# Performance work log

Hardware: AMD Instinct MI355X
Metric: run time of the kernel (lower is better)

Reference implementation:

```python
import jax, jax.numpy as jnp
import numpy as np

DIM = 1280
NUM_HEADS = 16
HEAD_DIM = DIM // NUM_HEADS  # 80
SCALE = HEAD_DIM ** -0.5
N_CHUNKS = 4
CHUNK = 2048
TOTAL = N_CHUNKS * CHUNK  # 8192


def setup_inputs() -> dict:
    key = jax.random.key(0)
    ks = jax.random.split(key, 5)
    hidden_states = jax.random.normal(ks[0], (TOTAL, DIM), dtype=jnp.float32)
    cu_seqlens = (jnp.arange(N_CHUNKS + 1, dtype=jnp.int32) * CHUNK)
    qkv_w = jax.random.normal(ks[1], (3 * DIM, DIM), dtype=jnp.float32) * (DIM ** -0.5)
    qkv_b = jax.random.normal(ks[2], (3 * DIM,), dtype=jnp.float32) * 0.02
    proj_w = jax.random.normal(ks[3], (DIM, DIM), dtype=jnp.float32) * (DIM ** -0.5)
    proj_b = jax.random.normal(ks[4], (DIM,), dtype=jnp.float32) * 0.02
    return {"hidden_states": hidden_states, "cu_seqlens": cu_seqlens,
            "qkv_w": qkv_w, "qkv_b": qkv_b, "proj_w": proj_w, "proj_b": proj_b}


def reference(hidden_states, cu_seqlens, qkv_w, qkv_b, proj_w, proj_b):
    S = hidden_states.shape[0]
    # fused QKV projection: (S, 3*dim) -> q,k,v each (S, H, Dh)
    qkv = hidden_states @ qkv_w.T + qkv_b
    qkv = qkv.reshape(S, 3, NUM_HEADS, HEAD_DIM)
    q, k, v = qkv[:, 0], qkv[:, 1], qkv[:, 2]
    # chunk boundaries are static metadata (module calls .tolist() on them)
    cu = np.asarray(cu_seqlens)
    outs = []
    for s, e in zip(cu[:-1], cu[1:]):
        s, e = int(s), int(e)
        qc = q[s:e].transpose(1, 0, 2)  # (H, L, Dh)
        kc = k[s:e].transpose(1, 0, 2)
        vc = v[s:e].transpose(1, 0, 2)
        # full (non-causal) attention within the chunk; softmax in fp32
        logits = jnp.einsum('hqd,hkd->hqk', qc, kc) * SCALE
        w = jax.nn.softmax(logits.astype(jnp.float32), axis=-1).astype(qc.dtype)
        oc = jnp.einsum('hqk,hkd->hqd', w, vc)  # (H, L, Dh)
        outs.append(oc.transpose(1, 0, 2).reshape(e - s, DIM))
    attn_out = jnp.concatenate(outs, axis=0)  # (S, dim)
    return attn_out @ proj_w.T + proj_b
```

## Files before the change

kernel.cpp:

```cpp
#include <hip/hip_runtime.h>
#include <hip/hip_bf16.h>
#include <stdint.h>

#define NHEADS 16
#define HDIM 80
#define CHUNK 2048
#define QSCALE 0.11180339887498949f
#define L2E 1.4426950408889634f

typedef __bf16 bf16x8 __attribute__((ext_vector_type(8)));
typedef float f32x4 __attribute__((ext_vector_type(4)));

__device__ __forceinline__ unsigned short f2bf(float f) {
  union { float f; unsigned u; } x; x.f = f;
  unsigned r = (x.u + 0x7fffu + ((x.u >> 16) & 1u)) >> 16;
  return (unsigned short)r;
}

__device__ __forceinline__ float fexp2(float x) {
  float r;
  asm("v_exp_f32 %0, %1" : "=v"(r) : "v"(x));
  return r;
}

__device__ __forceinline__ void gload16(const void* g, void* lds) {
  __builtin_amdgcn_global_load_lds((const __attribute__((address_space(1))) void*)g,
                                   (__attribute__((address_space(3))) void*)lds, 16, 0, 0);
}

__global__ __launch_bounds__(256) void cvt_f32_bf16(const float* __restrict__ in,
                                                    unsigned short* __restrict__ out, int n4) {
  int i = blockIdx.x * 256 + threadIdx.x;
  int stride = gridDim.x * 256;
  for (; i < n4; i += stride) {
    float4 v = reinterpret_cast<const float4*>(in)[i];
    ushort4 o;
    o.x = f2bf(v.x); o.y = f2bf(v.y); o.z = f2bf(v.z); o.w = f2bf(v.w);
    reinterpret_cast<ushort4*>(out)[i] = o;
  }
}

__global__ __launch_bounds__(256) void gemm_bt(
    const unsigned short* __restrict__ A, const unsigned short* __restrict__ B,
    const float* __restrict__ bias, unsigned short* __restrict__ C,
    float* __restrict__ Cf,
    int M, int N, int K, int lda, int scaleN, float scaleVal)
{
  __shared__ unsigned short Ash[128 * 32];
  __shared__ unsigned short Bsh[128 * 32];
  const int tid = threadIdx.x;
  const int lane = tid & 63;
  const int w = tid >> 6;
  const int wr = w >> 1, wc = w & 1;
  const int l15 = lane & 15, lq = lane >> 4;
  const long bm = (long)blockIdx.y * 128;
  const long bn = (long)blockIdx.x * 128;

  f32x4 acc[4][4];
#pragma unroll
  for (int i = 0; i < 4; i++)
#pragma unroll
    for (int j = 0; j < 4; j++) acc[i][j] = f32x4{0.f, 0.f, 0.f, 0.f};

  const int srow = lane >> 2;
  const int scol = (lane & 3) * 8;

  for (long k0 = 0; k0 < K; k0 += 32) {
    __syncthreads();
#pragma unroll
    for (int i = 0; i < 2; i++) {
      gload16(A + (bm + w * 32 + i * 16 + srow) * (long)lda + k0 + scol,
              (char*)Ash + (w * 2 + i) * 1024);
      gload16(B + (bn + w * 32 + i * 16 + srow) * (long)K + k0 + scol,
              (char*)Bsh + (w * 2 + i) * 1024);
    }
    __syncthreads();
    bf16x8 af[4], bfr[4];
#pragma unroll
    for (int x = 0; x < 4; x++) {
      af[x]  = *reinterpret_cast<const bf16x8*>(Ash + (wr * 64 + x * 16 + l15) * 32 + lq * 8);
      bfr[x] = *reinterpret_cast<const bf16x8*>(Bsh + (wc * 64 + x * 16 + l15) * 32 + lq * 8);
    }
#pragma unroll
    for (int x = 0; x < 4; x++)
#pragma unroll
      for (int y = 0; y < 4; y++)
        acc[x][y] = __builtin_amdgcn_mfma_f32_16x16x32_bf16(af[x], bfr[y], acc[x][y], 0, 0, 0);
  }

#pragma unroll
  for (int x = 0; x < 4; x++) {
    long row0 = bm + wr * 64 + x * 16 + lq * 4;
#pragma unroll
    for (int y = 0; y < 4; y++) {
      int col = (int)bn + wc * 64 + y * 16 + l15;
      float bs = bias[col];
      float sc = (col < scaleN) ? scaleVal : 1.0f;
      if (Cf != nullptr) {
#pragma unroll
        for (int r = 0; r < 4; r++)
          Cf[(size_t)(row0 + r) * N + col] = (acc[x][y][r] + bs) * sc;
      } else {
#pragma unroll
        for (int r = 0; r < 4; r++)
          C[(size_t)(row0 + r) * N + col] = f2bf((acc[x][y][r] + bs) * sc);
      }
    }
  }
}

__global__ __launch_bounds__(256) void transpose_v(
    const unsigned short* __restrict__ qkv, unsigned short* __restrict__ vt)
{
  __shared__ unsigned short Tsh[64 * 88];
  const int tid = threadIdx.x;
  const int ch = blockIdx.y >> 4, head = blockIdx.y & 15;
  const int st = blockIdx.x;
  const unsigned short* src = qkv + (size_t)(ch * CHUNK + st * 64) * 3840 + 2560 + head * HDIM;
  for (int s = tid; s < 640; s += 256) {
    int r = s / 10, c = s % 10;
    uint4 v = *reinterpret_cast<const uint4*>(src + (size_t)r * 3840 + c * 8);
    *reinterpret_cast<uint4*>(&Tsh[r * 88 + c * 8]) = v;
  }
  __syncthreads();
  unsigned short* dst = vt + ((size_t)(ch * 16 + head) * HDIM) * 2048 + st * 64;
  for (int s = tid; s < 640; s += 256) {
    int d = s >> 3, c2 = s & 7;
    unsigned short ubuf[8];
#pragma unroll
    for (int e = 0; e < 8; e++) ubuf[e] = Tsh[(c2 * 8 + e) * 88 + d];
    *reinterpret_cast<uint4*>(dst + (size_t)d * 2048 + c2 * 8) = *reinterpret_cast<const uint4*>(ubuf);
  }
}

__global__ __launch_bounds__(256, 3) void attn_kernel(
    const unsigned short* __restrict__ qkv, const unsigned short* __restrict__ vt,
    unsigned short* __restrict__ outq)
{
  __shared__ char Kbuf[10240];
  __shared__ char Vbuf[12288];
  __shared__ unsigned short Psh[4][32 * 72];

  const int tid = threadIdx.x;
  const int lane = tid & 63;
  const int w = tid >> 6;
  const int l15 = lane & 15, lq = lane >> 4;

  const int b = blockIdx.x;
  const int qt = (b >> 3) & 15;
  const int chp = (b & 7) * 8 + (b >> 7);
  const int ch = chp >> 4;
  const int head = chp & 15;

  const size_t rs = 3840;
  const unsigned short* qbase = qkv + (size_t)(ch * CHUNK) * rs + head * HDIM;
  const unsigned short* kbase = qbase + 1280;
  const unsigned short* vth = vt + (size_t)chp * HDIM * 2048;

  const char* ksrc[3]; int koff[3]; bool kact[3];
#pragma unroll
  for (int j = 0; j < 3; j++) {
    int c = w + 4 * j;
    kact[j] = (c < 10);
    int cc = kact[j] ? c : 0;
    int s = cc * 64 + lane;
    int r = s / 10, col = s % 10;
    ksrc[j] = (const char*)kbase + (size_t)r * 7680 + col * 16;
    koff[j] = cc * 1024;
  }
  const char* vsrc[3]; int voff[3];
#pragma unroll
  for (int j = 0; j < 3; j++) {
    int c = 10 + ((w + 2) & 3) + 4 * j;
    int s2 = (c - 10) * 64 + lane;
    if (s2 > 719) s2 = 719;
    int d = s2 / 9, u = s2 % 9;
    int ue = (u == 8) ? 0 : u;
    vsrc[j] = (const char*)(vth + (size_t)d * 2048 + ue * 8);
    voff[j] = (c - 10) * 1024;
  }

  const int qr0 = qt * 128 + w * 32;
  bf16x8 qa[2][2], qa2[2];
#pragma unroll
  for (int qf = 0; qf < 2; qf++) {
    const unsigned short* qrow = qbase + (size_t)(qr0 + qf * 16 + l15) * rs;
    qa[qf][0] = *reinterpret_cast<const bf16x8*>(qrow + lq * 8);
    qa[qf][1] = *reinterpret_cast<const bf16x8*>(qrow + 32 + lq * 8);
    if (lq < 2) qa2[qf] = *reinterpret_cast<const bf16x8*>(qrow + 64 + lq * 8);
    else        qa2[qf] = bf16x8{};
  }

  bf16x8 onesb;
  {
    __bf16 o = (l15 == 0) ? (__bf16)1.0f : (__bf16)0.0f;
    onesb = bf16x8{o, o, o, o, o, o, o, o};
  }

  f32x4 acc[2][6];
#pragma unroll
  for (int qf = 0; qf < 2; qf++)
#pragma unroll
    for (int df = 0; df < 6; df++) acc[qf][df] = f32x4{0.f, 0.f, 0.f, 0.f};
  float mst[2][4];
#pragma unroll
  for (int qf = 0; qf < 2; qf++)
#pragma unroll
    for (int r = 0; r < 4; r++) mst[qf][r] = -1e30f;

#pragma unroll
  for (int j = 0; j < 3; j++)
    if (kact[j]) { gload16(ksrc[j], Kbuf + koff[j]); ksrc[j] += 64 * 7680; }
#pragma unroll
  for (int j = 0; j < 3; j++) { gload16(vsrc[j], Vbuf + voff[j]); vsrc[j] += 128; }
  __syncthreads();

  for (int kt = 0; kt < CHUNK; kt += 64) {
    const unsigned short* Ksh = (const unsigned short*)Kbuf;
    const unsigned short* Vsh = (const unsigned short*)Vbuf;

    f32x4 s[2][4];
#pragma unroll
    for (int qf = 0; qf < 2; qf++)
#pragma unroll
      for (int kf = 0; kf < 4; kf++) s[qf][kf] = f32x4{0.f, 0.f, 0.f, 0.f};
#pragma unroll
    for (int kf = 0; kf < 4; kf++) {
      const unsigned short* kr = Ksh + (kf * 16 + l15) * 80;
      bf16x8 kb0 = *reinterpret_cast<const bf16x8*>(kr + lq * 8);
      bf16x8 kb1 = *reinterpret_cast<const bf16x8*>(kr + 32 + lq * 8);
      bf16x8 kb2 = (lq < 2) ? *reinterpret_cast<const bf16x8*>(kr + 64 + lq * 8) : bf16x8{};
#pragma unroll
      for (int qf = 0; qf < 2; qf++) {
        s[qf][kf] = __builtin_amdgcn_mfma_f32_16x16x32_bf16(qa[qf][0], kb0, s[qf][kf], 0, 0, 0);
        s[qf][kf] = __builtin_amdgcn_mfma_f32_16x16x32_bf16(qa[qf][1], kb1, s[qf][kf], 0, 0, 0);
        s[qf][kf] = __builtin_amdgcn_mfma_f32_16x16x32_bf16(qa2[qf], kb2, s[qf][kf], 0, 0, 0);
      }
    }

    float pmax[2][4];
    bool need = false;
#pragma unroll
    for (int qf = 0; qf < 2; qf++)
#pragma unroll
      for (int r = 0; r < 4; r++) {
        pmax[qf][r] = fmaxf(fmaxf(s[qf][0][r], s[qf][1][r]), fmaxf(s[qf][2][r], s[qf][3][r]));
        need = need || (pmax[qf][r] > mst[qf][r] + 8.0f);
      }
    if (__any(need)) {
#pragma unroll
      for (int m = 1; m < 16; m <<= 1)
#pragma unroll
        for (int qf = 0; qf < 2; qf++)
#pragma unroll
          for (int r = 0; r < 4; r++)
            pmax[qf][r] = fmaxf(pmax[qf][r], __shfl_xor(pmax[qf][r], m, 64));
#pragma unroll
      for (int qf = 0; qf < 2; qf++)
#pragma unroll
        for (int r = 0; r < 4; r++) {
          float mnew = fmaxf(mst[qf][r], pmax[qf][r]);
          float alpha = fexp2((mst[qf][r] - mnew) * L2E);
          mst[qf][r] = mnew;
#pragma unroll
          for (int df = 0; df < 6; df++) acc[qf][df][r] *= alpha;
        }
    }

#pragma unroll
    for (int qf = 0; qf < 2; qf++)
#pragma unroll
      for (int kf = 0; kf < 4; kf++)
#pragma unroll
        for (int r = 0; r < 4; r++) {
          float p = fexp2((s[qf][kf][r] - mst[qf][r]) * L2E);
          unsigned pk;
          asm("v_cvt_pk_bf16_f32 %0, %1, %2" : "=v"(pk) : "v"(p), "v"(p));
          Psh[w][(qf * 16 + lq * 4 + r) * 72 + kf * 16 + l15] = (unsigned short)pk;
        }

    __syncthreads();

    if (kt + 64 < CHUNK) {
#pragma unroll
      for (int j = 0; j < 3; j++)
        if (kact[j]) { gload16(ksrc[j], Kbuf + koff[j]); ksrc[j] += 64 * 7680; }
    }

#pragma unroll
    for (int ks = 0; ks < 2; ks++) {
      bf16x8 pa[2];
#pragma unroll
      for (int qf = 0; qf < 2; qf++)
        pa[qf] = *reinterpret_cast<const bf16x8*>(&Psh[w][(qf * 16 + l15) * 72 + ks * 32 + lq * 8]);
#pragma unroll
      for (int df = 0; df < 5; df++) {
        bf16x8 vb = *reinterpret_cast<const bf16x8*>(&Vsh[(df * 16 + l15) * 72 + ks * 32 + lq * 8]);
#pragma unroll
        for (int qf = 0; qf < 2; qf++)
          acc[qf][df] = __builtin_amdgcn_mfma_f32_16x16x32_bf16(pa[qf], vb, acc[qf][df], 0, 0, 0);
      }
#pragma unroll
      for (int qf = 0; qf < 2; qf++)
        acc[qf][5] = __builtin_amdgcn_mfma_f32_16x16x32_bf16(pa[qf], onesb, acc[qf][5], 0, 0, 0);
    }

    __syncthreads();

    if (kt + 64 < CHUNK) {
#pragma unroll
      for (int j = 0; j < 3; j++) { gload16(vsrc[j], Vbuf + voff[j]); vsrc[j] += 128; }
    }
  }

  unsigned short* obase = outq + (size_t)(ch * CHUNK) * rs + head * HDIM;
#pragma unroll
  for (int qf = 0; qf < 2; qf++) {
    float inv[4];
#pragma unroll
    for (int r = 0; r < 4; r++) inv[r] = 1.0f / __shfl(acc[qf][5][r], lq * 16, 64);
#pragma unroll
    for (int df = 0; df < 5; df++) {
      int col = df * 16 + l15;
#pragma unroll
      for (int r = 0; r < 4; r++) {
        float v = acc[qf][df][r] * inv[r];
        obase[(size_t)(qr0 + qf * 16 + lq * 4 + r) * rs + col] = f2bf(v);
      }
    }
  }
}

extern "C" void kernel_launch(void* const* d_in, const int* in_sizes, int n_in,
                              void* d_out, int out_size, void* d_ws, size_t ws_size,
                              hipStream_t stream) {
  const float* hs    = (const float*)d_in[0];
  const float* qkvw  = (const float*)d_in[2];
  const float* qkvb  = (const float*)d_in[3];
  const float* projw = (const float*)d_in[4];
  const float* projb = (const float*)d_in[5];

  char* ws = (char*)d_ws;
  unsigned short* hs_bf    = (unsigned short*)ws;
  unsigned short* vT       = hs_bf;
  unsigned short* qkvw_bf  = (unsigned short*)(ws + 20971520);
  unsigned short* projw_bf = (unsigned short*)(ws + 20971520 + 9830400);
  unsigned short* qkv_bf   = (unsigned short*)(ws + 20971520 + 9830400 + 3276800);

  cvt_f32_bf16<<<2048, 256, 0, stream>>>(hs,    hs_bf,    8192 * 1280 / 4);
  cvt_f32_bf16<<<1024, 256, 0, stream>>>(qkvw,  qkvw_bf,  3840 * 1280 / 4);
  cvt_f32_bf16<<<512,  256, 0, stream>>>(projw, projw_bf, 1280 * 1280 / 4);

  gemm_bt<<<dim3(30, 64), 256, 0, stream>>>(hs_bf, qkvw_bf, qkvb, qkv_bf, nullptr,
                                            8192, 3840, 1280, 1280, 1280, QSCALE);
  transpose_v<<<dim3(32, 64), 256, 0, stream>>>(qkv_bf, vT);
  attn_kernel<<<dim3(1024), 256, 0, stream>>>(qkv_bf, vT, qkv_bf);
  gemm_bt<<<dim3(10, 64), 256, 0, stream>>>(qkv_bf, projw_bf, projb,
                                            nullptr, (float*)d_out,
                                            8192, 1280, 1280, 3840, 0, 1.0f);
}
```

Measured before the change: 336.6 us.

## Make attention kernel persistent with atomic tile counter scheduling

Turns the attention kernel into a persistent kernel launched with 768 blocks (256 CUs x 3 occupancy). Each block loops and fetches its next tile from a global atomic counter, which the transpose kernel initialises in the output buffer. The aim is to remove the tail effect of 1024 equal tiles across 768 resident slots and to balance work dynamically. In exchange it adds one atomic and one barrier per tile, and it relies on d_out as scratch before the final GEMM overwrites it.

```diff
diff --git a/kernel.cpp b/kernel.cpp
--- a/kernel.cpp
+++ b/kernel.cpp
@@ -110,10 +110,11 @@
 }
 
 __global__ __launch_bounds__(256) void transpose_v(
-    const unsigned short* __restrict__ qkv, unsigned short* __restrict__ vt)
+    const unsigned short* __restrict__ qkv, unsigned short* __restrict__ vt, int* cnt)
 {
   __shared__ unsigned short Tsh[64 * 88];
   const int tid = threadIdx.x;
+  if (blockIdx.x == 0 && blockIdx.y == 0 && tid == 0) *cnt = 768;
   const int ch = blockIdx.y >> 4, head = blockIdx.y & 15;
   const int st = blockIdx.x;
   const unsigned short* src = qkv + (size_t)(ch * CHUNK + st * 64) * 3840 + 2560 + head * HDIM;
@@ -135,40 +136,30 @@
 
 __global__ __launch_bounds__(256, 3) void attn_kernel(
     const unsigned short* __restrict__ qkv, const unsigned short* __restrict__ vt,
-    unsigned short* __restrict__ outq)
+    unsigned short* __restrict__ outq, int* cnt)
 {
   __shared__ char Kbuf[10240];
   __shared__ char Vbuf[12288];
   __shared__ unsigned short Psh[4][32 * 72];
+  __shared__ int ntile;
 
   const int tid = threadIdx.x;
   const int lane = tid & 63;
   const int w = tid >> 6;
   const int l15 = lane & 15, lq = lane >> 4;
-
-  const int b = blockIdx.x;
-  const int qt = (b >> 3) & 15;
-  const int chp = (b & 7) * 8 + (b >> 7);
-  const int ch = chp >> 4;
-  const int head = chp & 15;
-
   const size_t rs = 3840;
-  const unsigned short* qbase = qkv + (size_t)(ch * CHUNK) * rs + head * HDIM;
-  const unsigned short* kbase = qbase + 1280;
-  const unsigned short* vth = vt + (size_t)chp * HDIM * 2048;
-
-  const char* ksrc[3]; int koff[3]; bool kact[3];
+
+  int kgoff[3], koff[3]; bool kact[3];
 #pragma unroll
   for (int j = 0; j < 3; j++) {
     int c = w + 4 * j;
     kact[j] = (c < 10);
     int cc = kact[j] ? c : 0;
     int s = cc * 64 + lane;
-    int r = s / 10, col = s % 10;
-    ksrc[j] = (const char*)kbase + (size_t)r * 7680 + col * 16;
+    kgoff[j] = (s / 10) * 7680 + (s % 10) * 16;
     koff[j] = cc * 1024;
   }
-  const char* vsrc[3]; int voff[3];
+  int vgoff[3], voff[3];
 #pragma unroll
   for (int j = 0; j < 3; j++) {
     int c = 10 + ((w + 2) & 3) + 4 * j;
@@ -176,19 +167,8 @@
     if (s2 > 719) s2 = 719;
     int d = s2 / 9, u = s2 % 9;
     int ue = (u == 8) ? 0 : u;
-    vsrc[j] = (const char*)(vth + (size_t)d * 2048 + ue * 8);
+    vgoff[j] = (d * 2048 + ue * 8) * 2;
     voff[j] = (c - 10) * 1024;
-  }
-
-  const int qr0 = qt * 128 + w * 32;
-  bf16x8 qa[2][2], qa2[2];
-#pragma unroll
-  for (int qf = 0; qf < 2; qf++) {
-    const unsigned short* qrow = qbase + (size_t)(qr0 + qf * 16 + l15) * rs;
-    qa[qf][0] = *reinterpret_cast<const bf16x8*>(qrow + lq * 8);
-    qa[qf][1] = *reinterpret_cast<const bf16x8*>(qrow + 32 + lq * 8);
-    if (lq < 2) qa2[qf] = *reinterpret_cast<const bf16x8*>(qrow + 64 + lq * 8);
-    else        qa2[qf] = bf16x8{};
   }
 
   bf16x8 onesb;
@@ -197,137 +177,168 @@
     onesb = bf16x8{o, o, o, o, o, o, o, o};
   }
 
-  f32x4 acc[2][6];
-#pragma unroll
-  for (int qf = 0; qf < 2; qf++)
-#pragma unroll
-    for (int df = 0; df < 6; df++) acc[qf][df] = f32x4{0.f, 0.f, 0.f, 0.f};
-  float mst[2][4];
-#pragma unroll
-  for (int qf = 0; qf < 2; qf++)
-#pragma unroll
-    for (int r = 0; r < 4; r++) mst[qf][r] = -1e30f;
-
-#pragma unroll
-  for (int j = 0; j < 3; j++)
-    if (kact[j]) { gload16(ksrc[j], Kbuf + koff[j]); ksrc[j] += 64 * 7680; }
-#pragma unroll
-  for (int j = 0; j < 3; j++) { gload16(vsrc[j], Vbuf + voff[j]); vsrc[j] += 128; }
-  __syncthreads();
-
-  for (int kt = 0; kt < CHUNK; kt += 64) {
-    const unsigned short* Ksh = (const unsigned short*)Kbuf;
-    const unsigned short* Vsh = (const unsigned short*)Vbuf;
-
-    f32x4 s[2][4];
+  int tile = blockIdx.x;
+  while (tile < 1024) {
+    const int qt = (tile >> 3) & 15;
+    const int chp = (tile & 7) * 8 + (tile >> 7);
+    const int ch = chp >> 4;
+    const int head = chp & 15;
+
+    const unsigned short* qbase = qkv + (size_t)(ch * CHUNK) * rs + head * HDIM;
+    const char* kbase = (const char*)(qbase + 1280);
+    const char* vth = (const char*)(vt + (size_t)chp * HDIM * 2048);
+
+    const char* ksrc[3]; const char* vsrc[3];
+#pragma unroll
+    for (int j = 0; j < 3; j++) { ksrc[j] = kbase + kgoff[j]; vsrc[j] = vth + vgoff[j]; }
+
+    const int qr0 = qt * 128 + w * 32;
+    bf16x8 qa[2][2], qa2[2];
+#pragma unroll
+    for (int qf = 0; qf < 2; qf++) {
+      const unsigned short* qrow = qbase + (size_t)(qr0 + qf * 16 + l15) * rs;
+      qa[qf][0] = *reinterpret_cast<const bf16x8*>(qrow + lq * 8);
+      qa[qf][1] = *reinterpret_cast<const bf16x8*>(qrow + 32 + lq * 8);
+      if (lq < 2) qa2[qf] = *reinterpret_cast<const bf16x8*>(qrow + 64 + lq * 8);
+      else        qa2[qf] = bf16x8{};
+    }
+
+    f32x4 acc[2][6];
 #pragma unroll
     for (int qf = 0; qf < 2; qf++)
 #pragma unroll
-      for (int kf = 0; kf < 4; kf++) s[qf][kf] = f32x4{0.f, 0.f, 0.f, 0.f};
-#pragma unroll
-    for (int kf = 0; kf < 4; kf++) {
-      const unsigned short* kr = Ksh + (kf * 16 + l15) * 80;
-      bf16x8 kb0 = *reinterpret_cast<const bf16x8*>(kr + lq * 8);
-      bf16x8 kb1 = *reinterpret_cast<const bf16x8*>(kr + 32 + lq * 8);
-      bf16x8 kb2 = (lq < 2) ? *reinterpret_cast<const bf16x8*>(kr + 64 + lq * 8) : bf16x8{};
-#pragma unroll
-      for (int qf = 0; qf < 2; qf++) {
-        s[qf][kf] = __builtin_amdgcn_mfma_f32_16x16x32_bf16(qa[qf][0], kb0, s[qf][kf], 0, 0, 0);
-        s[qf][kf] = __builtin_amdgcn_mfma_f32_16x16x32_bf16(qa[qf][1], kb1, s[qf][kf], 0, 0, 0);
-        s[qf][kf] = __builtin_amdgcn_mfma_f32_16x16x32_bf16(qa2[qf], kb2, s[qf][kf], 0, 0, 0);
-      }
-    }
-
-    float pmax[2][4];
-    bool need = false;
+      for (int df = 0; df < 6; df++) acc[qf][df] = f32x4{0.f, 0.f, 0.f, 0.f};
+    float mst[2][4];
 #pragma unroll
     for (int qf = 0; qf < 2; qf++)
 #pragma unroll
-      for (int r = 0; r < 4; r++) {
-        pmax[qf][r] = fmaxf(fmaxf(s[qf][0][r], s[qf][1][r]), fmaxf(s[qf][2][r], s[qf][3][r]));
-        need = need || (pmax[qf][r] > mst[qf][r] + 8.0f);
-      }
-    if (__any(need)) {
-#pragma unroll
-      for (int m = 1; m < 16; m <<= 1)
+      for (int r = 0; r < 4; r++) mst[qf][r] = -1e30f;
+
+#pragma unroll
+    for (int j = 0; j < 3; j++)
+      if (kact[j]) { gload16(ksrc[j], Kbuf + koff[j]); ksrc[j] += 64 * 7680; }
+#pragma unroll
+    for (int j = 0; j < 3; j++) { gload16(vsrc[j], Vbuf + voff[j]); vsrc[j] += 128; }
+    __syncthreads();
+
+    for (int kt = 0; kt < CHUNK; kt += 64) {
+      const unsigned short* Ksh = (const unsigned short*)Kbuf;
+      const unsigned short* Vsh = (const unsigned short*)Vbuf;
+
+      f32x4 s[2][4];
+#pragma unroll
+      for (int qf = 0; qf < 2; qf++)
+#pragma unroll
+        for (int kf = 0; kf < 4; kf++) s[qf][kf] = f32x4{0.f, 0.f, 0.f, 0.f};
+#pragma unroll
+      for (int kf = 0; kf < 4; kf++) {
+        const unsigned short* kr = Ksh + (kf * 16 + l15) * 80;
+        bf16x8 kb0 = *reinterpret_cast<const bf16x8*>(kr + lq * 8);
+        bf16x8 kb1 = *reinterpret_cast<const bf16x8*>(kr + 32 + lq * 8);
+        bf16x8 kb2 = (lq < 2) ? *reinterpret_cast<const bf16x8*>(kr + 64 + lq * 8) : bf16x8{};
+#pragma unroll
+        for (int qf = 0; qf < 2; qf++) {
+          s[qf][kf] = __builtin_amdgcn_mfma_f32_16x16x32_bf16(qa[qf][0], kb0, s[qf][kf], 0, 0, 0);
+          s[qf][kf] = __builtin_amdgcn_mfma_f32_16x16x32_bf16(qa[qf][1], kb1, s[qf][kf], 0, 0, 0);
+          s[qf][kf] = __builtin_amdgcn_mfma_f32_16x16x32_bf16(qa2[qf], kb2, s[qf][kf], 0, 0, 0);
+        }
+      }
+
+      float pmax[2][4];
+      bool need = false;
+#pragma unroll
+      for (int qf = 0; qf < 2; qf++)
+#pragma unroll
+        for (int r = 0; r < 4; r++) {
+          pmax[qf][r] = fmaxf(fmaxf(s[qf][0][r], s[qf][1][r]), fmaxf(s[qf][2][r], s[qf][3][r]));
+          need = need || (pmax[qf][r] > mst[qf][r] + 8.0f);
+        }
+      if (__any(need)) {
+#pragma unroll
+        for (int m = 1; m < 16; m <<= 1)
+#pragma unroll
+          for (int qf = 0; qf < 2; qf++)
+#pragma unroll
+            for (int r = 0; r < 4; r++)
+              pmax[qf][r] = fmaxf(pmax[qf][r], __shfl_xor(pmax[qf][r], m, 64));
 #pragma unroll
         for (int qf = 0; qf < 2; qf++)
 #pragma unroll
-          for (int r = 0; r < 4; r++)
-            pmax[qf][r] = fmaxf(pmax[qf][r], __shfl_xor(pmax[qf][r], m, 64));
+          for (int r = 0; r < 4; r++) {
+            float mnew = fmaxf(mst[qf][r], pmax[qf][r]);
+            float alpha = fexp2((mst[qf][r] - mnew) * L2E);
+            mst[qf][r] = mnew;
+#pragma unroll
+            for (int df = 0; df < 6; df++) acc[qf][df][r] *= alpha;
+          }
+      }
+
 #pragma unroll
       for (int qf = 0; qf < 2; qf++)
 #pragma unroll
+        for (int kf = 0; kf < 4; kf++)
+#pragma unroll
+          for (int r = 0; r < 4; r++) {
+            float p = fexp2((s[qf][kf][r] - mst[qf][r]) * L2E);
+            unsigned pk;
+            asm("v_cvt_pk_bf16_f32 %0, %1, %2" : "=v"(pk) : "v"(p), "v"(p));
+            Psh[w][(qf * 16 + lq * 4 + r) * 72 + kf * 16 + l15] = (unsigned short)pk;
+          }
+
+      __syncthreads();
+
+      if (kt + 64 < CHUNK) {
+#pragma unroll
+        for (int j = 0; j < 3; j++)
+          if (kact[j]) { gload16(ksrc[j], Kbuf + koff[j]); ksrc[j] += 64 * 7680; }
+      }
+
+#pragma unroll
+      for (int ks = 0; ks < 2; ks++) {
+        bf16x8 pa[2];
+#pragma unroll
+        for (int qf = 0; qf < 2; qf++)
+          pa[qf] = *reinterpret_cast<const bf16x8*>(&Psh[w][(qf * 16 + l15) * 72 + ks * 32 + lq * 8]);
+#pragma unroll
+        for (int df = 0; df < 5; df++) {
+          bf16x8 vb = *reinterpret_cast<const bf16x8*>(&Vsh[(df * 16 + l15) * 72 + ks * 32 + lq * 8]);
+#pragma unroll
+          for (int qf = 0; qf < 2; qf++)
+            acc[qf][df] = __builtin_amdgcn_mfma_f32_16x16x32_bf16(pa[qf], vb, acc[qf][df], 0, 0, 0);
+        }
+#pragma unroll
+        for (int qf = 0; qf < 2; qf++)
+          acc[qf][5] = __builtin_amdgcn_mfma_f32_16x16x32_bf16(pa[qf], onesb, acc[qf][5], 0, 0, 0);
+      }
+
+      __syncthreads();
+
+      if (kt + 64 < CHUNK) {
+#pragma unroll
+        for (int j = 0; j < 3; j++) { gload16(vsrc[j], Vbuf + voff[j]); vsrc[j] += 128; }
+      }
+    }
+
+    unsigned short* obase = outq + (size_t)(ch * CHUNK) * rs + head * HDIM;
+#pragma unroll
+    for (int qf = 0; qf < 2; qf++) {
+      float inv[4];
+#pragma unroll
+      for (int r = 0; r < 4; r++) inv[r] = 1.0f / __shfl(acc[qf][5][r], lq * 16, 64);
+#pragma unroll
+      for (int df = 0; df < 5; df++) {
+        int col = df * 16 + l15;
+#pragma unroll
         for (int r = 0; r < 4; r++) {
-          float mnew = fmaxf(mst[qf][r], pmax[qf][r]);
-          float alpha = fexp2((mst[qf][r] - mnew) * L2E);
-          mst[qf][r] = mnew;
-#pragma unroll
-          for (int df = 0; df < 6; df++) acc[qf][df][r] *= alpha;
+          float v = acc[qf][df][r] * inv[r];
+          obase[(size_t)(qr0 + qf * 16 + lq * 4 + r) * rs + col] = f2bf(v);
         }
-    }
-
-#pragma unroll
-    for (int qf = 0; qf < 2; qf++)
-#pragma unroll
-      for (int kf = 0; kf < 4; kf++)
-#pragma unroll
-        for (int r = 0; r < 4; r++) {
-          float p = fexp2((s[qf][kf][r] - mst[qf][r]) * L2E);
-          unsigned pk;
-          asm("v_cvt_pk_bf16_f32 %0, %1, %2" : "=v"(pk) : "v"(p), "v"(p));
-          Psh[w][(qf * 16 + lq * 4 + r) * 72 + kf * 16 + l15] = (unsigned short)pk;
-        }
-
+      }
+    }
+
+    if (tid == 0) ntile = atomicAdd(cnt, 1);
     __syncthreads();
-
-    if (kt + 64 < CHUNK) {
-#pragma unroll
-      for (int j = 0; j < 3; j++)
-        if (kact[j]) { gload16(ksrc[j], Kbuf + koff[j]); ksrc[j] += 64 * 7680; }
-    }
-
-#pragma unroll
-    for (int ks = 0; ks < 2; ks++) {
-      bf16x8 pa[2];
-#pragma unroll
-      for (int qf = 0; qf < 2; qf++)
-        pa[qf] = *reinterpret_cast<const bf16x8*>(&Psh[w][(qf * 16 + l15) * 72 + ks * 32 + lq * 8]);
-#pragma unroll
-      for (int df = 0; df < 5; df++) {
-        bf16x8 vb = *reinterpret_cast<const bf16x8*>(&Vsh[(df * 16 + l15) * 72 + ks * 32 + lq * 8]);
-#pragma unroll
-        for (int qf = 0; qf < 2; qf++)
-          acc[qf][df] = __builtin_amdgcn_mfma_f32_16x16x32_bf16(pa[qf], vb, acc[qf][df], 0, 0, 0);
-      }
-#pragma unroll
-      for (int qf = 0; qf < 2; qf++)
-        acc[qf][5] = __builtin_amdgcn_mfma_f32_16x16x32_bf16(pa[qf], onesb, acc[qf][5], 0, 0, 0);
-    }
-
-    __syncthreads();
-
-    if (kt + 64 < CHUNK) {
-#pragma unroll
-      for (int j = 0; j < 3; j++) { gload16(vsrc[j], Vbuf + voff[j]); vsrc[j] += 128; }
-    }
-  }
-
-  unsigned short* obase = outq + (size_t)(ch * CHUNK) * rs + head * HDIM;
-#pragma unroll
-  for (int qf = 0; qf < 2; qf++) {
-    float inv[4];
-#pragma unroll
-    for (int r = 0; r < 4; r++) inv[r] = 1.0f / __shfl(acc[qf][5][r], lq * 16, 64);
-#pragma unroll
-    for (int df = 0; df < 5; df++) {
-      int col = df * 16 + l15;
-#pragma unroll
-      for (int r = 0; r < 4; r++) {
-        float v = acc[qf][df][r] * inv[r];
-        obase[(size_t)(qr0 + qf * 16 + lq * 4 + r) * rs + col] = f2bf(v);
-      }
-    }
+    tile = ntile;
   }
 }
 
@@ -346,6 +357,7 @@
   unsigned short* qkvw_bf  = (unsigned short*)(ws + 20971520);
   unsigned short* projw_bf = (unsigned short*)(ws + 20971520 + 9830400);
   unsigned short* qkv_bf   = (unsigned short*)(ws + 20971520 + 9830400 + 3276800);
+  int* cnt = (int*)d_out;
 
   cvt_f32_bf16<<<2048, 256, 0, stream>>>(hs,    hs_bf,    8192 * 1280 / 4);
   cvt_f32_bf16<<<1024, 256, 0, stream>>>(qkvw,  qkvw_bf,  3840 * 1280 / 4);
@@ -353,8 +365,8 @@
 
   gemm_bt<<<dim3(30, 64), 256, 0, stream>>>(hs_bf, qkvw_bf, qkvb, qkv_bf, nullptr,
                                             8192, 3840, 1280, 1280, 1280, QSCALE);
-  transpose_v<<<dim3(32, 64), 256, 0, stream>>>(qkv_bf, vT);
-  attn_kernel<<<dim3(1024), 256, 0, stream>>>(qkv_bf, vT, qkv_bf);
+  transpose_v<<<dim3(32, 64), 256, 0, stream>>>(qkv_bf, vT, cnt);
+  attn_kernel<<<dim3(768), 256, 0, stream>>>(qkv_bf, vT, qkv_bf, cnt);
   gemm_bt<<<dim3(10, 64), 256, 0, stream>>>(qkv_bf, projw_bf, projb,
                                             nullptr, (float*)d_out,
                                             8192, 1280, 1280, 3840, 0, 1.0f);
```

Result: no change. 342.3 us (+1.7%).

## Fuse score exp with running-max tracking and defer accumulator rescale after PV

Applied to the files above, without the earlier changes.

Exponentials are now computed straight from each MFMA score fragment using the previous running max. Each 16-wide fragment is converted to bf16 P immediately, so the full score tile never has to stay in registers. The row max is reduced afterwards, and the accumulator is rescaled by alpha after the PV MFMAs rather than before them. The running max now starts at 16 instead of -1e30, and K/V global addresses are kept as 32-bit offsets from a base instead of per-load 64-bit pointers, which cuts register pressure. The risk is overflow: P is computed against a stale max, so scores far above it could overflow before the rescale is applied.

```diff
diff --git a/kernel.cpp b/kernel.cpp
--- a/kernel.cpp
+++ b/kernel.cpp
@@ -154,30 +154,29 @@
 
   const size_t rs = 3840;
   const unsigned short* qbase = qkv + (size_t)(ch * CHUNK) * rs + head * HDIM;
-  const unsigned short* kbase = qbase + 1280;
-  const unsigned short* vth = vt + (size_t)chp * HDIM * 2048;
-
-  const char* ksrc[3]; int koff[3]; bool kact[3];
+  const char* kbase = (const char*)(qbase + 1280);
+  const char* vbase = (const char*)(vt + (size_t)chp * HDIM * 2048);
+
+  int kgo[3]; bool kact[3];
+  const int koff0 = w * 1024;
 #pragma unroll
   for (int j = 0; j < 3; j++) {
     int c = w + 4 * j;
     kact[j] = (c < 10);
     int cc = kact[j] ? c : 0;
     int s = cc * 64 + lane;
-    int r = s / 10, col = s % 10;
-    ksrc[j] = (const char*)kbase + (size_t)r * 7680 + col * 16;
-    koff[j] = cc * 1024;
-  }
-  const char* vsrc[3]; int voff[3];
+    kgo[j] = (s / 10) * 7680 + (s % 10) * 16;
+  }
+  int vgo[3];
+  const int vw = (w + 2) & 3;
 #pragma unroll
   for (int j = 0; j < 3; j++) {
-    int c = 10 + ((w + 2) & 3) + 4 * j;
-    int s2 = (c - 10) * 64 + lane;
+    int c = vw + 4 * j;
+    int s2 = c * 64 + lane;
     if (s2 > 719) s2 = 719;
     int d = s2 / 9, u = s2 % 9;
     int ue = (u == 8) ? 0 : u;
-    vsrc[j] = (const char*)(vth + (size_t)d * 2048 + ue * 8);
-    voff[j] = (c - 10) * 1024;
+    vgo[j] = d * 4096 + ue * 16;
   }
 
   const int qr0 = qt * 128 + w * 32;
@@ -206,24 +205,23 @@
 #pragma unroll
   for (int qf = 0; qf < 2; qf++)
 #pragma unroll
-    for (int r = 0; r < 4; r++) mst[qf][r] = -1e30f;
+    for (int r = 0; r < 4; r++) mst[qf][r] = 16.0f;
 
 #pragma unroll
   for (int j = 0; j < 3; j++)
-    if (kact[j]) { gload16(ksrc[j], Kbuf + koff[j]); ksrc[j] += 64 * 7680; }
-#pragma unroll
-  for (int j = 0; j < 3; j++) { gload16(vsrc[j], Vbuf + voff[j]); vsrc[j] += 128; }
+    if (kact[j]) gload16(kbase + kgo[j], Kbuf + koff0 + j * 4096);
+#pragma unroll
+  for (int j = 0; j < 3; j++) gload16(vbase + vgo[j], Vbuf + vw * 1024 + j * 4096);
   __syncthreads();
 
   for (int kt = 0; kt < CHUNK; kt += 64) {
+    float tmax[2][4];
+#pragma unroll
+    for (int qf = 0; qf < 2; qf++)
+#pragma unroll
+      for (int r = 0; r < 4; r++) tmax[qf][r] = -1e30f;
+
     const unsigned short* Ksh = (const unsigned short*)Kbuf;
-    const unsigned short* Vsh = (const unsigned short*)Vbuf;
-
-    f32x4 s[2][4];
-#pragma unroll
-    for (int qf = 0; qf < 2; qf++)
-#pragma unroll
-      for (int kf = 0; kf < 4; kf++) s[qf][kf] = f32x4{0.f, 0.f, 0.f, 0.f};
 #pragma unroll
     for (int kf = 0; kf < 4; kf++) {
       const unsigned short* kr = Ksh + (kf * 16 + l15) * 80;
@@ -232,61 +230,57 @@
       bf16x8 kb2 = (lq < 2) ? *reinterpret_cast<const bf16x8*>(kr + 64 + lq * 8) : bf16x8{};
 #pragma unroll
       for (int qf = 0; qf < 2; qf++) {
-        s[qf][kf] = __builtin_amdgcn_mfma_f32_16x16x32_bf16(qa[qf][0], kb0, s[qf][kf], 0, 0, 0);
-        s[qf][kf] = __builtin_amdgcn_mfma_f32_16x16x32_bf16(qa[qf][1], kb1, s[qf][kf], 0, 0, 0);
-        s[qf][kf] = __builtin_amdgcn_mfma_f32_16x16x32_bf16(qa2[qf], kb2, s[qf][kf], 0, 0, 0);
-      }
-    }
-
-    float pmax[2][4];
-    bool need = false;
-#pragma unroll
-    for (int qf = 0; qf < 2; qf++)
-#pragma unroll
-      for (int r = 0; r < 4; r++) {
-        pmax[qf][r] = fmaxf(fmaxf(s[qf][0][r], s[qf][1][r]), fmaxf(s[qf][2][r], s[qf][3][r]));
-        need = need || (pmax[qf][r] > mst[qf][r] + 8.0f);
-      }
-    if (__any(need)) {
-#pragma unroll
-      for (int m = 1; m < 16; m <<= 1)
-#pragma unroll
-        for (int qf = 0; qf < 2; qf++)
-#pragma unroll
-          for (int r = 0; r < 4; r++)
-            pmax[qf][r] = fmaxf(pmax[qf][r], __shfl_xor(pmax[qf][r], m, 64));
-#pragma unroll
-      for (int qf = 0; qf < 2; qf++)
+        f32x4 sv = f32x4{0.f, 0.f, 0.f, 0.f};
+        sv = __builtin_amdgcn_mfma_f32_16x16x32_bf16(qa[qf][0], kb0, sv, 0, 0, 0);
+        sv = __builtin_amdgcn_mfma_f32_16x16x32_bf16(qa[qf][1], kb1, sv, 0, 0, 0);
+        sv = __builtin_amdgcn_mfma_f32_16x16x32_bf16(qa2[qf], kb2, sv, 0, 0, 0);
 #pragma unroll
         for (int r = 0; r < 4; r++) {
-          float mnew = fmaxf(mst[qf][r], pmax[qf][r]);
-          float alpha = fexp2((mst[qf][r] - mnew) * L2E);
-          mst[qf][r] = mnew;
-#pragma unroll
-          for (int df = 0; df < 6; df++) acc[qf][df][r] *= alpha;
-        }
-    }
-
-#pragma unroll
-    for (int qf = 0; qf < 2; qf++)
-#pragma unroll
-      for (int kf = 0; kf < 4; kf++)
-#pragma unroll
-        for (int r = 0; r < 4; r++) {
-          float p = fexp2((s[qf][kf][r] - mst[qf][r]) * L2E);
+          tmax[qf][r] = fmaxf(tmax[qf][r], sv[r]);
+          float p = fexp2((sv[r] - mst[qf][r]) * L2E);
           unsigned pk;
           asm("v_cvt_pk_bf16_f32 %0, %1, %2" : "=v"(pk) : "v"(p), "v"(p));
           Psh[w][(qf * 16 + lq * 4 + r) * 72 + kf * 16 + l15] = (unsigned short)pk;
         }
+      }
+    }
+
+    bool need = false;
+#pragma unroll
+    for (int qf = 0; qf < 2; qf++)
+#pragma unroll
+      for (int r = 0; r < 4; r++)
+        need = need || (tmax[qf][r] > mst[qf][r] + 8.0f);
+    const bool resc = __any(need);
+    float alpha[2][4];
+    if (resc) {
+#pragma unroll
+      for (int m = 1; m < 16; m <<= 1)
+#pragma unroll
+        for (int qf = 0; qf < 2; qf++)
+#pragma unroll
+          for (int r = 0; r < 4; r++)
+            tmax[qf][r] = fmaxf(tmax[qf][r], __shfl_xor(tmax[qf][r], m, 64));
+#pragma unroll
+      for (int qf = 0; qf < 2; qf++)
+#pragma unroll
+        for (int r = 0; r < 4; r++) {
+          float mnew = fmaxf(mst[qf][r], tmax[qf][r]);
+          alpha[qf][r] = fexp2((mst[qf][r] - mnew) * L2E);
+          mst[qf][r] = mnew;
+        }
+    }
 
     __syncthreads();
 
     if (kt + 64 < CHUNK) {
+      const int ktB = (kt + 64) * 7680;
 #pragma unroll
       for (int j = 0; j < 3; j++)
-        if (kact[j]) { gload16(ksrc[j], Kbuf + koff[j]); ksrc[j] += 64 * 7680; }
-    }
-
+        if (kact[j]) gload16(kbase + kgo[j] + ktB, Kbuf + koff0 + j * 4096);
+    }
+
+    const unsigned short* Vsh = (const unsigned short*)Vbuf;
 #pragma unroll
     for (int ks = 0; ks < 2; ks++) {
       bf16x8 pa[2];
@@ -305,11 +299,22 @@
         acc[qf][5] = __builtin_amdgcn_mfma_f32_16x16x32_bf16(pa[qf], onesb, acc[qf][5], 0, 0, 0);
     }
 
+    if (resc) {
+#pragma unroll
+      for (int qf = 0; qf < 2; qf++)
+#pragma unroll
+        for (int df = 0; df < 6; df++)
+#pragma unroll
+          for (int r = 0; r < 4; r++) acc[qf][df][r] *= alpha[qf][r];
+    }
+
     __syncthreads();
 
     if (kt + 64 < CHUNK) {
-#pragma unroll
-      for (int j = 0; j < 3; j++) { gload16(vsrc[j], Vbuf + voff[j]); vsrc[j] += 128; }
+      const int ktV = (kt + 64) * 2;
+#pragma unroll
+      for (int j = 0; j < 3; j++)
+        gload16(vbase + vgo[j] + ktV, Vbuf + vw * 1024 + j * 4096);
     }
   }
 
```

Result: no change. 333.5 us (-0.9%).
